# Optimization experiments

Hardware: AMD Instinct MI355X
Metric: run time of the kernel (lower is better)

The kernel has to match this reference:

```python
import jax, jax.numpy as jnp
import numpy as np

KF_TOTAL = 196   # hw*hw, keyframe tokens
KF_KEEP = 147
INCR_KEEP = 49


def _l2norm(v, eps=1e-12):
    n = jnp.linalg.norm(v, axis=-1, keepdims=True)
    return v / jnp.maximum(n, eps)


def _kf_guided_compress(x):
    # x: (B, 4*196, D)
    B, T, D = x.shape
    kf = x[:, :KF_TOTAL, :]          # (B, 196, D)
    incr = x[:, KF_TOTAL:, :]        # (B, 588, D)

    kf_n = _l2norm(kf)
    sim_kf = jnp.einsum('bic,bjc->bij', kf_n, kf_n)      # (B,196,196)
    redundancy = sim_kf.sum(axis=-1) - 1.0                # (B,196)
    sorted_idx = jnp.argsort(redundancy, axis=-1)         # ascending
    keep_kf_idx = jnp.sort(sorted_idx[:, :KF_KEEP], axis=-1)
    kf_sum = jnp.take_along_axis(kf, keep_kf_idx[:, :, None], axis=1)  # (B,147,D)
    kf_count = jnp.ones((B, KF_KEEP, 1), dtype=x.dtype)

    bidx = jnp.arange(B)[:, None]
    n_incr = incr.shape[1]
    # Loop schedule is fully determined by static shapes -> Python unroll is jit-safe.
    while n_incr > INCR_KEEP:
        n_to_merge = min(n_incr // 3, n_incr - INCR_KEEP)
        if n_to_merge <= 0:
            break
        kf_avg = kf_sum / kf_count
        sim_cross = jnp.einsum('bkc,bic->bki', _l2norm(kf_avg), _l2norm(incr))  # (B,147,n_incr)
        max_sim = sim_cross.max(axis=1)      # (B, n_incr)
        best_kf = sim_cross.argmax(axis=1)   # (B, n_incr)
        rank = jnp.argsort(-max_sim, axis=-1)            # descending
        merge_idx = rank[:, :n_to_merge]
        keep_idx_incr = jnp.sort(rank[:, n_to_merge:], axis=-1)
        target_kf = jnp.take_along_axis(best_kf, merge_idx, axis=1)        # (B, m)
        merge_feats = jnp.take_along_axis(incr, merge_idx[:, :, None], axis=1)  # (B,m,D)
        kf_sum = kf_sum.at[bidx, target_kf].add(merge_feats)
        kf_count = kf_count.at[bidx, target_kf].add(jnp.ones((B, n_to_merge, 1), x.dtype))
        incr = jnp.take_along_axis(incr, keep_idx_incr[:, :, None], axis=1)
        n_incr -= n_to_merge

    kf_final = kf_sum / kf_count
    return jnp.concatenate([kf_final, incr], axis=1)   # (B, 196, D)


def setup_inputs() -> dict:
    key = jax.random.key(0)
    ks = jax.random.split(key, 3)
    F_, N, D, H = 256, 196, 1024, 4096
    x = jax.random.normal(ks[0], (F_, N, D), dtype=jnp.float32)
    w1 = jax.random.normal(ks[1], (D, H), dtype=jnp.float32) * 0.02
    b1 = jnp.zeros((H,), dtype=jnp.float32)
    w2 = jax.random.normal(ks[2], (H, H), dtype=jnp.float32) * 0.02
    b2 = jnp.zeros((H,), dtype=jnp.float32)
    return {"x": x, "w1": w1, "b1": b1, "w2": w2, "b2": b2, "local_num_frames": 4}


def reference(x, w1, b1, w2, b2, local_num_frames):
    F_, N, D = x.shape
    n_clips = F_ // local_num_frames
    xc = x.reshape(n_clips, local_num_frames * N, D)
    z = _kf_guided_compress(xc)                    # (n_clips, 196, D)
    h = jax.nn.gelu(jnp.einsum('bnd,dh->bnh', z, w1) + b1, approximate=False)
    out = jnp.einsum('bnh,hk->bnk', h, w2) + b2    # (n_clips, 196, hidden)
    return out
```

## Files before the change

### kernel.cpp

```cpp
#include <hip/hip_runtime.h>
#include <math.h>

typedef __bf16 bf16;
typedef __bf16 bf16x8 __attribute__((ext_vector_type(8)));
typedef float f32x4 __attribute__((ext_vector_type(4)));

#define DEV static __device__ __forceinline__

constexpr int NB    = 64;
constexpr int TCLIP = 784;
constexpr int TKF   = 196;
constexpr int KKEEP = 147;
constexpr int NINC0 = 588;
constexpr int DIM   = 1024;
constexpr int MR    = NB * TKF;
constexpr int NH    = 4096;

constexpr size_t OFF_W1T  = 0;
constexpr size_t OFF_W2T  = OFF_W1T  + (size_t)NH*DIM*2;
constexpr size_t OFF_Z    = OFF_W2T  + (size_t)NH*NH*2;
constexpr size_t OFF_H    = OFF_Z    + (size_t)MR*DIM*2;
constexpr size_t OFF_KFS  = OFF_H    + (size_t)MR*NH*2;
constexpr size_t OFF_KFC  = OFF_KFS  + (size_t)NB*KKEEP*DIM*4;
constexpr size_t OFF_INV  = OFF_KFC  + (size_t)NB*KKEEP*4;
constexpr size_t OFF_S    = OFF_INV  + (size_t)NB*TCLIP*8;
constexpr size_t OFF_RED  = OFF_S    + (size_t)NB*DIM*8;
constexpr size_t OFF_KSRC = OFF_RED  + (size_t)NB*TKF*4;
constexpr size_t OFF_IDXA = OFF_KSRC + (size_t)NB*KKEEP*4;
constexpr size_t OFF_IDXB = OFF_IDXA + (size_t)NB*NINC0*4;
constexpr size_t OFF_MAXS = OFF_IDXB + (size_t)NB*NINC0*4;
constexpr size_t OFF_BK   = OFF_MAXS + (size_t)NB*NINC0*4;
constexpr size_t OFF_MSRC = OFF_BK   + (size_t)NB*NINC0*4;
constexpr size_t OFF_MTGT = OFF_MSRC + (size_t)NB*TKF*4;
constexpr size_t KFA_ELT  = (size_t)NB * KKEEP * DIM;

__global__ void k_transpose_bf16(const float* __restrict__ in, bf16* __restrict__ out,
                                 int R, int C) {
  __shared__ float t[32][33];
  int c0 = blockIdx.x * 32, r0 = blockIdx.y * 32;
  int tx = threadIdx.x, ty = threadIdx.y;
#pragma unroll
  for (int i = 0; i < 4; i++) t[ty + 8*i][tx] = in[(size_t)(r0 + ty + 8*i) * C + c0 + tx];
  __syncthreads();
#pragma unroll
  for (int i = 0; i < 4; i++)
    out[(size_t)(c0 + ty + 8*i) * R + r0 + tx] = (bf16)t[tx][ty + 8*i];
}

__global__ void k_row_invnorm(const float* __restrict__ x, double* __restrict__ invn) {
  __shared__ double sm[256];
  int row = blockIdx.x, tid = threadIdx.x;
  const float* p = x + (size_t)row * DIM;
  double a = 0.0;
  for (int c = tid; c < DIM; c += 256) { double v = p[c]; a += v * v; }
  sm[tid] = a; __syncthreads();
#pragma unroll
  for (int s = 128; s >= 1; s >>= 1) { if (tid < s) sm[tid] += sm[tid + s]; __syncthreads(); }
  if (tid == 0) invn[row] = 1.0 / fmax(sqrt(sm[0]), 1e-12);
}

__global__ void k_kf_colsum(const float* __restrict__ x, const double* __restrict__ invn,
                            double* __restrict__ S) {
  int b = blockIdx.x, tid = threadIdx.x;
  __shared__ double iv[TKF];
  for (int i = tid; i < TKF; i += 256) iv[i] = invn[b * TCLIP + i];
  __syncthreads();
  for (int c = tid; c < DIM; c += 256) {
    double s = 0.0;
    for (int i = 0; i < TKF; i++) {
      float kn = (float)((double)x[((size_t)b * TCLIP + i) * DIM + c] * iv[i]);
      s += (double)kn;
    }
    S[b * DIM + c] = s;
  }
}

__global__ void k_redundancy(const float* __restrict__ x, const double* __restrict__ invn,
                             const double* __restrict__ S, float* __restrict__ red) {
  __shared__ double sm[256];
  int i = blockIdx.x, b = blockIdx.y, tid = threadIdx.x;
  const float* p = x + ((size_t)b * TCLIP + i) * DIM;
  double iv = invn[b * TCLIP + i];
  double a = 0.0;
  for (int c = tid; c < DIM; c += 256) {
    float kn = (float)((double)p[c] * iv);
    a += (double)kn * S[b * DIM + c];
  }
  sm[tid] = a; __syncthreads();
#pragma unroll
  for (int s = 128; s >= 1; s >>= 1) { if (tid < s) sm[tid] += sm[tid + s]; __syncthreads(); }
  if (tid == 0) red[b * TKF + i] = (float)(sm[0] - 1.0);
}

__global__ void k_select_kf(const float* __restrict__ red, int* __restrict__ kf_src,
                            float* __restrict__ kfcnt, int* __restrict__ idxA) {
  __shared__ float r[TKF];
  __shared__ int keep[TKF];
  int b = blockIdx.x, tid = threadIdx.x;
  if (tid < TKF) r[tid] = red[b * TKF + tid];
  __syncthreads();
  if (tid < TKF) {
    float ri = r[tid]; int rank = 0;
    for (int j = 0; j < TKF; j++) rank += (r[j] < ri) + ((j < tid) && (r[j] == ri));
    keep[tid] = rank < KKEEP;
  }
  __syncthreads();
  if (tid < TKF && keep[tid]) {
    int pos = 0;
    for (int j = 0; j < tid; j++) pos += keep[j];
    kf_src[b * KKEEP + pos] = tid;
  }
  if (tid < KKEEP) kfcnt[b * KKEEP + tid] = 1.0f;
  for (int u = tid; u < NINC0; u += 256) idxA[b * NINC0 + u] = u;
}

__global__ void k_gather_kf(const float* __restrict__ x, const int* __restrict__ kf_src,
                            float* __restrict__ kfsum) {
  int k = blockIdx.x, b = blockIdx.y, tid = threadIdx.x;
  int sr = kf_src[b * KKEEP + k];
  const float* s = x + ((size_t)b * TCLIP + sr) * DIM;
  float* d = kfsum + ((size_t)b * KKEEP + k) * DIM;
  for (int c = tid; c < DIM; c += 256) d[c] = s[c];
}

__global__ void k_kfa(const float* __restrict__ kfsum, const float* __restrict__ kfcnt,
                      bf16* __restrict__ khi, bf16* __restrict__ kmid,
                      bf16* __restrict__ klo) {
  __shared__ double sm[256];
  int k = blockIdx.x, b = blockIdx.y, tid = threadIdx.x;
  float cnt = kfcnt[b * KKEEP + k];
  size_t base = ((size_t)b * KKEEP + k) * DIM;
  const float* s = kfsum + base;
  float av[4]; double a = 0.0;
#pragma unroll
  for (int j = 0; j < 4; j++) { av[j] = s[tid + 256*j] / cnt; a += (double)av[j] * av[j]; }
  sm[tid] = a; __syncthreads();
#pragma unroll
  for (int sdt = 128; sdt >= 1; sdt >>= 1) { if (tid < sdt) sm[tid] += sm[tid + sdt]; __syncthreads(); }
  float nf = fmaxf((float)sqrt(sm[0]), 1e-12f);
#pragma unroll
  for (int j = 0; j < 4; j++) {
    float v = av[j] / nf;
    bf16 h = (bf16)v;
    float r1 = v - (float)h;
    bf16 m = (bf16)r1;
    float r2 = r1 - (float)m;
    khi[base + tid + 256*j]  = h;
    kmid[base + tid + 256*j] = m;
    klo[base + tid + 256*j]  = (bf16)r2;
  }
}

template <int NI>
__global__ __launch_bounds__(256) void k_sim_mfma(const float* __restrict__ x,
                                                  const double* __restrict__ invn,
                                                  const bf16* __restrict__ khi,
                                                  const bf16* __restrict__ kmid,
                                                  const bf16* __restrict__ klo,
                                                  const int* __restrict__ idx_cur,
                                                  float* __restrict__ max_sim,
                                                  int* __restrict__ best_kf) {
  __shared__ __align__(16) bf16 Ah[160 * 32];
  __shared__ __align__(16) bf16 Am[160 * 32];
  __shared__ __align__(16) bf16 Al[160 * 32];
  __shared__ __align__(16) bf16 Bh[64 * 32];
  __shared__ __align__(16) bf16 Bm[64 * 32];
  __shared__ __align__(16) bf16 Bl[64 * 32];
  __shared__ int toks[64];
  __shared__ double ivv[64];

  int b = blockIdx.y, p0 = blockIdx.x * 64, tid = threadIdx.x;
  int w = tid >> 6, l = tid & 63;

  if (tid < 64) {
    int p = p0 + tid;
    bool ok = p < NI;
    toks[tid] = ok ? idx_cur[b * NINC0 + p] : 0;
    ivv[tid] = ok ? invn[b * TCLIP + TKF + toks[tid]] : 0.0;
  }

  f32x4 acc[10];
#pragma unroll
  for (int t = 0; t < 10; t++) acc[t] = f32x4{0.f, 0.f, 0.f, 0.f};

  int brow = tid >> 2;
  int bko  = (tid & 3) * 8;
  size_t kbase = (size_t)b * KKEEP * DIM;

  for (int kk = 0; kk < DIM; kk += 32) {
    __syncthreads();
#pragma unroll
    for (int j = 0; j < 3; j++) {
      int c = tid + 256 * j;
      if (c < 640) {
        int row = c >> 2, off8 = (c & 3) * 8;
        uint4 vh = {0,0,0,0}, vm = {0,0,0,0}, vl = {0,0,0,0};
        if (row < KKEEP) {
          size_t g = kbase + (size_t)row * DIM + kk + off8;
          vh = *(const uint4*)(khi + g);
          vm = *(const uint4*)(kmid + g);
          vl = *(const uint4*)(klo + g);
        }
        *(uint4*)(Ah + row * 32 + off8) = vh;
        *(uint4*)(Am + row * 32 + off8) = vm;
        *(uint4*)(Al + row * 32 + off8) = vl;
      }
    }
    {
      const float* src = x + ((size_t)b * TCLIP + TKF + toks[brow]) * DIM + kk + bko;
      double iv = ivv[brow];
      float4 f0 = *(const float4*)src;
      float4 f1 = *(const float4*)(src + 4);
      float vv[8] = {f0.x, f0.y, f0.z, f0.w, f1.x, f1.y, f1.z, f1.w};
#pragma unroll
      for (int e = 0; e < 8; e++) {
        float v = (float)((double)vv[e] * iv);
        bf16 h = (bf16)v;
        float r1 = v - (float)h;
        bf16 m = (bf16)r1;
        float r2 = r1 - (float)m;
        int o = brow * 32 + bko + e;
        Bh[o] = h; Bm[o] = m; Bl[o] = (bf16)r2;
      }
    }
    __syncthreads();

    int fo = ((w * 16 + (l & 15)) << 5) + ((l >> 4) << 3);
    bf16x8 fbh = *(const bf16x8*)(Bh + fo);
    bf16x8 fbm = *(const bf16x8*)(Bm + fo);
    bf16x8 fbl = *(const bf16x8*)(Bl + fo);
#pragma unroll
    for (int t = 0; t < 10; t++) {
      int ao = ((t * 16 + (l & 15)) << 5) + ((l >> 4) << 3);
      bf16x8 fah = *(const bf16x8*)(Ah + ao);
      bf16x8 fam = *(const bf16x8*)(Am + ao);
      bf16x8 fal = *(const bf16x8*)(Al + ao);
      acc[t] = __builtin_amdgcn_mfma_f32_16x16x32_bf16(fah, fbh, acc[t], 0, 0, 0);
      acc[t] = __builtin_amdgcn_mfma_f32_16x16x32_bf16(fah, fbm, acc[t], 0, 0, 0);
      acc[t] = __builtin_amdgcn_mfma_f32_16x16x32_bf16(fam, fbh, acc[t], 0, 0, 0);
      acc[t] = __builtin_amdgcn_mfma_f32_16x16x32_bf16(fam, fbm, acc[t], 0, 0, 0);
      acc[t] = __builtin_amdgcn_mfma_f32_16x16x32_bf16(fah, fbl, acc[t], 0, 0, 0);
      acc[t] = __builtin_amdgcn_mfma_f32_16x16x32_bf16(fal, fbh, acc[t], 0, 0, 0);
    }
  }

  float vmax = -3.0e38f; int varg = 1 << 30;
  int g4 = (l >> 4) << 2;
#pragma unroll
  for (int t = 0; t < 10; t++) {
#pragma unroll
    for (int r = 0; r < 4; r++) {
      int row = t * 16 + g4 + r;
      float v = acc[t][r];
      if (row < KKEEP && v > vmax) { vmax = v; varg = row; }
    }
  }
#pragma unroll
  for (int off = 16; off <= 32; off <<= 1) {
    float ov = __shfl_xor(vmax, off, 64);
    int   oa = __shfl_xor(varg, off, 64);
    if (ov > vmax || (ov == vmax && oa < varg)) { vmax = ov; varg = oa; }
  }
  if (l < 16) {
    int p = p0 + w * 16 + l;
    if (p < NI) { max_sim[b * NINC0 + p] = vmax; best_kf[b * NINC0 + p] = varg; }
  }
}

template <int NI, int NM>
__global__ void k_rank_merge(const float* __restrict__ max_sim, const int* __restrict__ best_kf,
                             const int* __restrict__ idx_cur, int* __restrict__ idx_next,
                             int* __restrict__ msrc, int* __restrict__ mtgt) {
  __shared__ float s[NINC0];
  __shared__ short dr[NINC0];
  int b = blockIdx.x, tid = threadIdx.x;
  for (int i = tid; i < NI; i += 256) s[i] = max_sim[b * NINC0 + i];
  __syncthreads();
  for (int i = tid; i < NI; i += 256) {
    float si = s[i]; int cnt = 0;
    for (int j = 0; j < NI; j++) cnt += (s[j] > si) + ((j < i) && (s[j] == si));
    dr[i] = (short)cnt;
  }
  __syncthreads();
  for (int i = tid; i < NI; i += 256) {
    int r = dr[i];
    if (r < NM) {
      mtgt[b * TKF + r] = best_kf[b * NINC0 + i];
      msrc[b * TKF + r] = idx_cur[b * NINC0 + i];
    } else {
      int pos = 0;
      for (int j = 0; j < i; j++) pos += (dr[j] >= NM);
      idx_next[b * NINC0 + pos] = idx_cur[b * NINC0 + i];
    }
  }
}

template <int NM>
__global__ void k_merge(const float* __restrict__ x, const int* __restrict__ msrc,
                        const int* __restrict__ mtgt, float* __restrict__ kfsum,
                        float* __restrict__ kfcnt) {
  int k = blockIdx.x, b = blockIdx.y, tid = threadIdx.x;
  float* drow = kfsum + ((size_t)b * KKEEP + k) * DIM;
  float acc[4];
#pragma unroll
  for (int j = 0; j < 4; j++) acc[j] = drow[tid + 256*j];
  int adds = 0;
  for (int m = 0; m < NM; m++) {
    int tgt = mtgt[b * TKF + m];
    if (tgt == k) {
      int u = msrc[b * TKF + m];
      const float* r = x + ((size_t)b * TCLIP + TKF + u) * DIM;
#pragma unroll
      for (int j = 0; j < 4; j++) acc[j] += r[tid + 256*j];
      adds++;
    }
  }
#pragma unroll
  for (int j = 0; j < 4; j++) drow[tid + 256*j] = acc[j];
  if (tid == 0 && adds) kfcnt[b * KKEEP + k] += (float)adds;
}

__global__ void k_assemble_z(const float* __restrict__ x, const float* __restrict__ kfsum,
                             const float* __restrict__ kfcnt, const int* __restrict__ idx_fin,
                             bf16* __restrict__ z) {
  int r = blockIdx.x, b = blockIdx.y, tid = threadIdx.x;
  bf16* zr = z + ((size_t)b * TKF + r) * DIM;
  if (r < KKEEP) {
    float cnt = kfcnt[b * KKEEP + r];
    const float* s = kfsum + ((size_t)b * KKEEP + r) * DIM;
    for (int c = tid; c < DIM; c += 256) zr[c] = (bf16)(s[c] / cnt);
  } else {
    int u = idx_fin[b * NINC0 + (r - KKEEP)];
    const float* s = x + ((size_t)b * TCLIP + TKF + u) * DIM;
    for (int c = tid; c < DIM; c += 256) zr[c] = (bf16)s[c];
  }
}

DEV void gl2lds16(const bf16* g, bf16* l) {
  __builtin_amdgcn_global_load_lds((const __attribute__((address_space(1))) void*)g,
                                   (__attribute__((address_space(3))) void*)l, 16, 0, 0);
}

template <int EPI>
__global__ __launch_bounds__(256) void k_gemm_bt(const bf16* __restrict__ A,
                                                 const bf16* __restrict__ Bt,
                                                 const float* __restrict__ bias,
                                                 float* __restrict__ outF,
                                                 bf16* __restrict__ outB, int K) {
  __shared__ __align__(16) bf16 As[128 * 32];
  __shared__ __align__(16) bf16 Bs[128 * 32];
  int tid = threadIdx.x, w = tid >> 6, l = tid & 63;
  int m0 = blockIdx.x * 128, n0 = blockIdx.y * 128;
  int wr = w >> 1, wc = w & 1;
  f32x4 acc[4][4];
#pragma unroll
  for (int i = 0; i < 4; i++)
#pragma unroll
    for (int j = 0; j < 4; j++) acc[i][j] = f32x4{0.f, 0.f, 0.f, 0.f};

  int srow = w * 32 + (l >> 2);
  int scol = (l & 3) * 8;
  const bf16* gA = A + (size_t)(m0 + srow) * K + scol;
  const bf16* gB = Bt + (size_t)(n0 + srow) * K + scol;
  const size_t str16 = (size_t)16 * K;
  bf16* lA0 = As + (w * 32) * 32;
  bf16* lA1 = As + (w * 32 + 16) * 32;
  bf16* lB0 = Bs + (w * 32) * 32;
  bf16* lB1 = Bs + (w * 32 + 16) * 32;

  int fro = (l & 15), ko = (l >> 4) * 8;
  for (int kk = 0; kk < K; kk += 32) {
    __syncthreads();
    gl2lds16(gA + kk, lA0);
    gl2lds16(gA + kk + str16, lA1);
    gl2lds16(gB + kk, lB0);
    gl2lds16(gB + kk + str16, lB1);
    __syncthreads();
    bf16x8 af[4], bfr[4];
#pragma unroll
    for (int mi = 0; mi < 4; mi++)
      af[mi] = *(const bf16x8*)(As + (wr * 64 + mi * 16 + fro) * 32 + ko);
#pragma unroll
    for (int ni = 0; ni < 4; ni++)
      bfr[ni] = *(const bf16x8*)(Bs + (wc * 64 + ni * 16 + fro) * 32 + ko);
#pragma unroll
    for (int mi = 0; mi < 4; mi++)
#pragma unroll
      for (int ni = 0; ni < 4; ni++)
        acc[mi][ni] = __builtin_amdgcn_mfma_f32_16x16x32_bf16(af[mi], bfr[ni], acc[mi][ni], 0, 0, 0);
  }
  int col0 = n0 + wc * 64 + (l & 15);
  int row0 = m0 + wr * 64 + ((l >> 4) << 2);
#pragma unroll
  for (int ni = 0; ni < 4; ni++) {
    int col = col0 + ni * 16;
    float bv = bias[col];
#pragma unroll
    for (int mi = 0; mi < 4; mi++) {
#pragma unroll
      for (int r = 0; r < 4; r++) {
        int row = row0 + mi * 16 + r;
        float v = acc[mi][ni][r] + bv;
        if (EPI == 0) {
          float g = 0.5f * v * (1.0f + erff(v * 0.70710678118654752f));
          outB[(size_t)row * NH + col] = (bf16)g;
        } else {
          outF[(size_t)row * NH + col] = v;
        }
      }
    }
  }
}

template <int NI, int NM>
static void run_iter(const float* x, const double* INV, float* KFS, float* KFC,
                     bf16* KH, bf16* KM, bf16* KL,
                     const int* cur, int* next, float* MAXS, int* BK, int* MSRC, int* MTGT,
                     hipStream_t stream) {
  k_kfa<<<dim3(KKEEP, NB), 256, 0, stream>>>(KFS, KFC, KH, KM, KL);
  k_sim_mfma<NI><<<dim3((NI + 63) / 64, NB), 256, 0, stream>>>(x, INV, KH, KM, KL, cur, MAXS, BK);
  k_rank_merge<NI, NM><<<NB, 256, 0, stream>>>(MAXS, BK, cur, next, MSRC, MTGT);
  k_merge<NM><<<dim3(KKEEP, NB), 256, 0, stream>>>(x, MSRC, MTGT, KFS, KFC);
}

extern "C" void kernel_launch(void* const* d_in, const int* in_sizes, int n_in,
                              void* d_out, int out_size, void* d_ws, size_t ws_size,
                              hipStream_t stream) {
  const float* x  = (const float*)d_in[0];
  const float* w1 = (const float*)d_in[1];
  const float* b1 = (const float*)d_in[2];
  const float* w2 = (const float*)d_in[3];
  const float* b2 = (const float*)d_in[4];
  float* out = (float*)d_out;
  char* ws = (char*)d_ws;

  bf16*   W1T  = (bf16*)(ws + OFF_W1T);
  bf16*   W2T  = (bf16*)(ws + OFF_W2T);
  bf16*   Z    = (bf16*)(ws + OFF_Z);
  bf16*   H    = (bf16*)(ws + OFF_H);
  float*  KFS  = (float*)(ws + OFF_KFS);
  float*  KFC  = (float*)(ws + OFF_KFC);
  double* INV  = (double*)(ws + OFF_INV);
  double* S    = (double*)(ws + OFF_S);
  float*  RED  = (float*)(ws + OFF_RED);
  int*    KSRC = (int*)(ws + OFF_KSRC);
  int*    IDXA = (int*)(ws + OFF_IDXA);
  int*    IDXB = (int*)(ws + OFF_IDXB);
  float*  MAXS = (float*)(ws + OFF_MAXS);
  int*    BK   = (int*)(ws + OFF_BK);
  int*    MSRC = (int*)(ws + OFF_MSRC);
  int*    MTGT = (int*)(ws + OFF_MTGT);
  bf16*   KH   = (bf16*)(ws + OFF_H);
  bf16*   KM   = KH + KFA_ELT;
  bf16*   KL   = KM + KFA_ELT;

  k_transpose_bf16<<<dim3(NH / 32, DIM / 32), dim3(32, 8), 0, stream>>>(w1, W1T, DIM, NH);
  k_transpose_bf16<<<dim3(NH / 32, NH / 32), dim3(32, 8), 0, stream>>>(w2, W2T, NH, NH);

  k_row_invnorm<<<NB * TCLIP, 256, 0, stream>>>(x, INV);
  k_kf_colsum<<<NB, 256, 0, stream>>>(x, INV, S);
  k_redundancy<<<dim3(TKF, NB), 256, 0, stream>>>(x, INV, S, RED);
  k_select_kf<<<NB, 256, 0, stream>>>(RED, KSRC, KFC, IDXA);
  k_gather_kf<<<dim3(KKEEP, NB), 256, 0, stream>>>(x, KSRC, KFS);

  run_iter<588, 196>(x, INV, KFS, KFC, KH, KM, KL, IDXA, IDXB, MAXS, BK, MSRC, MTGT, stream);
  run_iter<392, 130>(x, INV, KFS, KFC, KH, KM, KL, IDXB, IDXA, MAXS, BK, MSRC, MTGT, stream);
  run_iter<262,  87>(x, INV, KFS, KFC, KH, KM, KL, IDXA, IDXB, MAXS, BK, MSRC, MTGT, stream);
  run_iter<175,  58>(x, INV, KFS, KFC, KH, KM, KL, IDXB, IDXA, MAXS, BK, MSRC, MTGT, stream);
  run_iter<117,  39>(x, INV, KFS, KFC, KH, KM, KL, IDXA, IDXB, MAXS, BK, MSRC, MTGT, stream);
  run_iter< 78,  26>(x, INV, KFS, KFC, KH, KM, KL, IDXB, IDXA, MAXS, BK, MSRC, MTGT, stream);
  run_iter< 52,   3>(x, INV, KFS, KFC, KH, KM, KL, IDXA, IDXB, MAXS, BK, MSRC, MTGT, stream);

  k_assemble_z<<<dim3(TKF, NB), 256, 0, stream>>>(x, KFS, KFC, IDXB, Z);

  k_gemm_bt<0><<<dim3(MR / 128, NH / 128), 256, 0, stream>>>(Z, W1T, b1, nullptr, H, DIM);
  k_gemm_bt<1><<<dim3(MR / 128, NH / 128), 256, 0, stream>>>(H, W2T, b2, out, nullptr, NH);
}
```

Before: 2.591 ms.

## Swizzle LDS tiles, group GEMM block order, and split kf colsum across blocks

Applies an XOR swizzle to the k-chunk placement in LDS, for both the cross-similarity kernel and the main GEMM, so fragment reads avoid bank conflicts. The B-tile stores become vectorized bf16x8 writes. The GEMM launch changes to a 1D grid with grouped (super-row) block ordering to improve L2 reuse of weight tiles. The keyframe column-sum kernel now uses four blocks per clip, one per 256-column slice, which raises parallelism from 64 blocks. The swizzle has to stay consistent between the global-load offsets and the fragment read offsets.

```diff
diff --git a/kernel.cpp b/kernel.cpp
--- a/kernel.cpp
+++ b/kernel.cpp
@@ -61,18 +61,17 @@
 
 __global__ void k_kf_colsum(const float* __restrict__ x, const double* __restrict__ invn,
                             double* __restrict__ S) {
-  int b = blockIdx.x, tid = threadIdx.x;
+  int b = blockIdx.x >> 2, tid = threadIdx.x;
+  int c = ((blockIdx.x & 3) << 8) + tid;
   __shared__ double iv[TKF];
   for (int i = tid; i < TKF; i += 256) iv[i] = invn[b * TCLIP + i];
   __syncthreads();
-  for (int c = tid; c < DIM; c += 256) {
-    double s = 0.0;
-    for (int i = 0; i < TKF; i++) {
-      float kn = (float)((double)x[((size_t)b * TCLIP + i) * DIM + c] * iv[i]);
-      s += (double)kn;
-    }
-    S[b * DIM + c] = s;
-  }
+  double s = 0.0;
+  for (int i = 0; i < TKF; i++) {
+    float kn = (float)((double)x[((size_t)b * TCLIP + i) * DIM + c] * iv[i]);
+    s += (double)kn;
+  }
+  S[b * DIM + c] = s;
 }
 
 __global__ void k_redundancy(const float* __restrict__ x, const double* __restrict__ invn,
@@ -184,7 +183,8 @@
   for (int t = 0; t < 10; t++) acc[t] = f32x4{0.f, 0.f, 0.f, 0.f};
 
   int brow = tid >> 2;
-  int bko  = (tid & 3) * 8;
+  int bk8g = ((tid & 3) ^ ((tid >> 3) & 3)) * 8;
+  int bcol = (tid & 3) * 8;
   size_t kbase = (size_t)b * KKEEP * DIM;
 
   for (int kk = 0; kk < DIM; kk += 32) {
@@ -193,25 +193,27 @@
     for (int j = 0; j < 3; j++) {
       int c = tid + 256 * j;
       if (c < 640) {
-        int row = c >> 2, off8 = (c & 3) * 8;
+        int row = c >> 2, cc = (c & 3);
+        int k8g = (cc ^ ((row >> 1) & 3)) * 8;
         uint4 vh = {0,0,0,0}, vm = {0,0,0,0}, vl = {0,0,0,0};
         if (row < KKEEP) {
-          size_t g = kbase + (size_t)row * DIM + kk + off8;
+          size_t g = kbase + (size_t)row * DIM + kk + k8g;
           vh = *(const uint4*)(khi + g);
           vm = *(const uint4*)(kmid + g);
           vl = *(const uint4*)(klo + g);
         }
-        *(uint4*)(Ah + row * 32 + off8) = vh;
-        *(uint4*)(Am + row * 32 + off8) = vm;
-        *(uint4*)(Al + row * 32 + off8) = vl;
+        *(uint4*)(Ah + row * 32 + cc * 8) = vh;
+        *(uint4*)(Am + row * 32 + cc * 8) = vm;
+        *(uint4*)(Al + row * 32 + cc * 8) = vl;
       }
     }
     {
-      const float* src = x + ((size_t)b * TCLIP + TKF + toks[brow]) * DIM + kk + bko;
+      const float* src = x + ((size_t)b * TCLIP + TKF + toks[brow]) * DIM + kk + bk8g;
       double iv = ivv[brow];
       float4 f0 = *(const float4*)src;
       float4 f1 = *(const float4*)(src + 4);
       float vv[8] = {f0.x, f0.y, f0.z, f0.w, f1.x, f1.y, f1.z, f1.w};
+      bf16x8 oh, om, ol;
 #pragma unroll
       for (int e = 0; e < 8; e++) {
         float v = (float)((double)vv[e] * iv);
@@ -219,19 +221,21 @@
         float r1 = v - (float)h;
         bf16 m = (bf16)r1;
         float r2 = r1 - (float)m;
-        int o = brow * 32 + bko + e;
-        Bh[o] = h; Bm[o] = m; Bl[o] = (bf16)r2;
+        oh[e] = h; om[e] = m; ol[e] = (bf16)r2;
       }
+      int o = brow * 32 + bcol;
+      *(bf16x8*)(Bh + o) = oh; *(bf16x8*)(Bm + o) = om; *(bf16x8*)(Bl + o) = ol;
     }
     __syncthreads();
 
-    int fo = ((w * 16 + (l & 15)) << 5) + ((l >> 4) << 3);
+    int ko_sw = (((l >> 4) ^ ((l >> 1) & 3)) << 3);
+    int fo = ((w * 16 + (l & 15)) << 5) + ko_sw;
     bf16x8 fbh = *(const bf16x8*)(Bh + fo);
     bf16x8 fbm = *(const bf16x8*)(Bm + fo);
     bf16x8 fbl = *(const bf16x8*)(Bl + fo);
 #pragma unroll
     for (int t = 0; t < 10; t++) {
-      int ao = ((t * 16 + (l & 15)) << 5) + ((l >> 4) << 3);
+      int ao = ((t * 16 + (l & 15)) << 5) + ko_sw;
       bf16x8 fah = *(const bf16x8*)(Ah + ao);
       bf16x8 fam = *(const bf16x8*)(Am + ao);
       bf16x8 fal = *(const bf16x8*)(Al + ao);
@@ -341,6 +345,10 @@
                                    (__attribute__((address_space(3))) void*)l, 16, 0, 0);
 }
 
+constexpr int GRM = MR / 128;
+constexpr int GRN = NH / 128;
+constexpr int GRP = 8;
+
 template <int EPI>
 __global__ __launch_bounds__(256) void k_gemm_bt(const bf16* __restrict__ A,
                                                  const bf16* __restrict__ Bt,
@@ -350,7 +358,16 @@
   __shared__ __align__(16) bf16 As[128 * 32];
   __shared__ __align__(16) bf16 Bs[128 * 32];
   int tid = threadIdx.x, w = tid >> 6, l = tid & 63;
-  int m0 = blockIdx.x * 128, n0 = blockIdx.y * 128;
+
+  int bid = blockIdx.x;
+  int nig = GRP * GRN;
+  int gid = bid / nig;
+  int fm = gid * GRP;
+  int gsz = min(GRP, GRM - fm);
+  int idx = bid % nig;
+  int m0 = (fm + idx % gsz) * 128;
+  int n0 = (idx / gsz) * 128;
+
   int wr = w >> 1, wc = w & 1;
   f32x4 acc[4][4];
 #pragma unroll
@@ -359,7 +376,7 @@
     for (int j = 0; j < 4; j++) acc[i][j] = f32x4{0.f, 0.f, 0.f, 0.f};
 
   int srow = w * 32 + (l >> 2);
-  int scol = (l & 3) * 8;
+  int scol = ((l & 3) ^ ((l >> 3) & 3)) * 8;
   const bf16* gA = A + (size_t)(m0 + srow) * K + scol;
   const bf16* gB = Bt + (size_t)(n0 + srow) * K + scol;
   const size_t str16 = (size_t)16 * K;
@@ -368,7 +385,8 @@
   bf16* lB0 = Bs + (w * 32) * 32;
   bf16* lB1 = Bs + (w * 32 + 16) * 32;
 
-  int fro = (l & 15), ko = (l >> 4) * 8;
+  int fro = (l & 15);
+  int ko_sw = (((l >> 4) ^ ((l >> 1) & 3)) << 3);
   for (int kk = 0; kk < K; kk += 32) {
     __syncthreads();
     gl2lds16(gA + kk, lA0);
@@ -379,10 +397,10 @@
     bf16x8 af[4], bfr[4];
 #pragma unroll
     for (int mi = 0; mi < 4; mi++)
-      af[mi] = *(const bf16x8*)(As + (wr * 64 + mi * 16 + fro) * 32 + ko);
+      af[mi] = *(const bf16x8*)(As + (wr * 64 + mi * 16 + fro) * 32 + ko_sw);
 #pragma unroll
     for (int ni = 0; ni < 4; ni++)
-      bfr[ni] = *(const bf16x8*)(Bs + (wc * 64 + ni * 16 + fro) * 32 + ko);
+      bfr[ni] = *(const bf16x8*)(Bs + (wc * 64 + ni * 16 + fro) * 32 + ko_sw);
 #pragma unroll
     for (int mi = 0; mi < 4; mi++)
 #pragma unroll
@@ -458,7 +476,7 @@
   k_transpose_bf16<<<dim3(NH / 32, NH / 32), dim3(32, 8), 0, stream>>>(w2, W2T, NH, NH);
 
   k_row_invnorm<<<NB * TCLIP, 256, 0, stream>>>(x, INV);
-  k_kf_colsum<<<NB, 256, 0, stream>>>(x, INV, S);
+  k_kf_colsum<<<NB * 4, 256, 0, stream>>>(x, INV, S);
   k_redundancy<<<dim3(TKF, NB), 256, 0, stream>>>(x, INV, S, RED);
   k_select_kf<<<NB, 256, 0, stream>>>(RED, KSRC, KFC, IDXA);
   k_gather_kf<<<dim3(KKEEP, NB), 256, 0, stream>>>(x, KSRC, KFS);
@@ -473,6 +491,6 @@
 
   k_assemble_z<<<dim3(TKF, NB), 256, 0, stream>>>(x, KFS, KFC, IDXB, Z);
 
-  k_gemm_bt<0><<<dim3(MR / 128, NH / 128), 256, 0, stream>>>(Z, W1T, b1, nullptr, H, DIM);
-  k_gemm_bt<1><<<dim3(MR / 128, NH / 128), 256, 0, stream>>>(H, W2T, b2, out, nullptr, NH);
-}
+  k_gemm_bt<0><<<GRM * GRN, 256, 0, stream>>>(Z, W1T, b1, nullptr, H, DIM);
+  k_gemm_bt<1><<<GRM * GRN, 256, 0, stream>>>(H, W2T, b2, out, nullptr, NH);
+}
```

Result: faster. 2.517 ms (-2.8%).
